# Kernel optimization log

Hardware: AMD Instinct MI355X
Metric: run time of the kernel (lower is better)

## Reference

```python
import jax, jax.numpy as jnp
import numpy as np

N, E, F_IN, H, C = 50000, 800000, 128, 4, 73
HC = H * C  # 292
NEG_SLOPE_ATT = 0.2   # GATv2 attention leaky relu
NEG_SLOPE_ACT = 0.01  # F.leaky_relu default
BN_EPS = 1e-5


def setup_inputs() -> dict:
    key = jax.random.key(0)
    ks = jax.random.split(key, 20)
    rn = lambda k, shp, s=0.05: (jax.random.normal(k, shp, jnp.float32) * s)
    inp = {
        'x': jax.random.normal(ks[0], (N, F_IN), jnp.float32),
        'edge_index': jax.random.randint(ks[1], (2, E), 0, N, jnp.int64),
        # conv1 (in=F_IN)
        'Wl1': rn(ks[2], (HC, F_IN)), 'bl1': rn(ks[3], (HC,)),
        'Wr1': rn(ks[4], (HC, F_IN)), 'br1': rn(ks[5], (HC,)),
        'att1': rn(ks[6], (H, C)), 'b1': rn(ks[7], (HC,)),
        # conv2 (in=HC)
        'Wl2': rn(ks[8], (HC, HC)), 'bl2': rn(ks[9], (HC,)),
        'Wr2': rn(ks[10], (HC, HC)), 'br2': rn(ks[11], (HC,)),
        'att2': rn(ks[12], (H, C)), 'b2': rn(ks[13], (HC,)),
        # shared BatchNorm1d(HC)
        'gamma': jnp.ones((HC,), jnp.float32), 'beta': jnp.zeros((HC,), jnp.float32),
        # classifier Linear(HC, 2)
        'Wc': rn(ks[14], (2, HC)), 'bc': rn(ks[15], (2,)),
    }
    return inp


def _gatv2(x, src, dst, Wl, bl, Wr, br, att, b):
    # lin_l on source, lin_r on target (PyG GATv2Conv, share_weights=False)
    xl = (x @ Wl.T + bl).reshape(-1, H, C)  # [N,H,C]
    xr = (x @ Wr.T + br).reshape(-1, H, C)
    f = xl[src] + xr[dst]                    # [E,H,C] edge-wise gather
    s = jnp.einsum('ehc,hc->eh', jax.nn.leaky_relu(f, NEG_SLOPE_ATT), att)
    # segment softmax over incoming edges of each destination node
    m = jax.ops.segment_max(s, dst, num_segments=N)
    ex = jnp.exp(s - m[dst])
    den = jax.ops.segment_sum(ex, dst, num_segments=N)
    alpha = ex / (den[dst] + 1e-16)          # [E,H]
    out = jax.ops.segment_sum(alpha[:, :, None] * xl[src], dst, num_segments=N)
    return out.reshape(-1, HC) + b           # concat heads + bias


def _bn(x, gamma, beta):
    mu = jnp.mean(x, axis=0)
    var = jnp.mean((x - mu) ** 2, axis=0)
    return (x - mu) * jax.lax.rsqrt(var + BN_EPS) * gamma + beta


def reference(x, edge_index, Wl1, bl1, Wr1, br1, att1, b1,
              Wl2, bl2, Wr2, br2, att2, b2, gamma, beta, Wc, bc):
    src, dst = edge_index[0], edge_index[1]
    h = _gatv2(x, src, dst, Wl1, bl1, Wr1, br1, att1, b1)
    h = jax.nn.leaky_relu(_bn(h, gamma, beta), NEG_SLOPE_ACT)
    h = _gatv2(h, src, dst, Wl2, bl2, Wr2, br2, att2, b2)
    h = jax.nn.leaky_relu(_bn(h, gamma, beta), NEG_SLOPE_ACT)
    return h @ Wc.T + bc
```

## Files before the change

kernel.cpp:

```cpp
#include <hip/hip_runtime.h>

#define HCDIM 292
#define NHEAD 4
#define CDIM 73
#define SLOTS 5
#define NPERM 320
#define BN_EPS 1e-5f
#define LOG2E 1.44269504f

using u16x8 = __attribute__((ext_vector_type(8))) unsigned short;
using f32x4 = __attribute__((ext_vector_type(4))) float;
using u16x4 = __attribute__((ext_vector_type(4))) unsigned short;
using hf2   = __attribute__((ext_vector_type(2))) _Float16;
using v2h   = __attribute__((ext_vector_type(2))) __fp16;
using v8h   = __attribute__((ext_vector_type(8))) __fp16;

__device__ inline v2h pkrtz(float a, float b) {
  return __builtin_amdgcn_cvt_pkrtz(a, b);
}
__device__ inline float fdot2(hf2 a, hf2 b, float c) {
  return __builtin_amdgcn_fdot2(__builtin_bit_cast(v2h, a),
                                __builtin_bit_cast(v2h, b), c, false);
}
__device__ inline ushort f2h(float f) {
  _Float16 h = (_Float16)f;
  return __builtin_bit_cast(ushort, h);
}
__device__ inline float h2f(ushort v) {
  return (float)__builtin_bit_cast(_Float16, v);
}
__device__ inline hf2 habs2(hf2 a) {
  unsigned u = __builtin_bit_cast(unsigned, a) & 0x7fff7fffu;
  return __builtin_bit_cast(hf2, u);
}
__device__ inline float fexp2(float x) {
  float r;
  asm("v_exp_f32 %0, %1" : "=v"(r) : "v"(x));
  return r;
}

#define FMAMIX_LO(ACC, W, U)                                                  \
  asm("v_fma_mix_f32 %0, %1, %2, %0 op_sel_hi:[1,0,0]"                        \
      : "+v"(ACC) : "v"(U), "v"(W))
#define FMAMIX_HI(ACC, W, U)                                                  \
  asm("v_fma_mix_f32 %0, %1, %2, %0 op_sel:[1,0,0] op_sel_hi:[1,0,0]"         \
      : "+v"(ACC) : "v"(U), "v"(W))

__device__ inline float dpp16_allsum(float v) {
  union { float f; int i; } a, b;
  a.f = v;
  b.i = __builtin_amdgcn_update_dpp(0, a.i, 0xB1, 0xf, 0xf, true);
  a.f += b.f;
  b.i = __builtin_amdgcn_update_dpp(0, a.i, 0x4E, 0xf, 0xf, true);
  a.f += b.f;
  b.i = __builtin_amdgcn_update_dpp(0, a.i, 0x124, 0xf, 0xf, true);
  a.f += b.f;
  b.i = __builtin_amdgcn_update_dpp(0, a.i, 0x128, 0xf, 0xf, true);
  a.f += b.f;
  return a.f;
}

__device__ inline int perm2feat(int p, bool& valid) {
  int h, c;
  if (p < 256) {
    h = p >> 6;
    c = ((p & 3) << 4) | ((p >> 2) & 15);
    valid = true;
  } else {
    int q = p - 256;
    h = q >> 4;
    c = 64 + (q & 15);
    valid = (q & 15) < (CDIM - 64);
  }
  return h * CDIM + c;
}

__global__ __launch_bounds__(320) void k_prep(
    const float* __restrict__ Wl1, const float* __restrict__ bl1,
    const float* __restrict__ Wr1, const float* __restrict__ br1,
    const float* __restrict__ Wl2, const float* __restrict__ bl2,
    const float* __restrict__ Wr2, const float* __restrict__ br2,
    ushort* __restrict__ wb1, float* __restrict__ pb1,
    ushort* __restrict__ wb2, float* __restrict__ pb2,
    const float* __restrict__ att1, const float* __restrict__ b1v,
    const float* __restrict__ att2, const float* __restrict__ b2v,
    const float* __restrict__ gamma, const float* __restrict__ beta,
    const float* __restrict__ Wc, float* __restrict__ vecp,
    const int* __restrict__ dst, int* __restrict__ deg, int E) {
  int bx = blockIdx.x, t = threadIdx.x;
  if (bx >= 5 * NPERM) {
    int i = (bx - 5 * NPERM) * 320 + t;
    int i4 = i * 4;
    if (i4 + 3 < E) {
      int4 d = *(const int4*)(dst + i4);
      atomicAdd(&deg[d.x], 1);
      atomicAdd(&deg[d.y], 1);
      atomicAdd(&deg[d.z], 1);
      atomicAdd(&deg[d.w], 1);
    } else {
      for (int k = i4; k < E; ++k) atomicAdd(&deg[dst[k]], 1);
    }
    return;
  }
  int seg = bx / NPERM;
  int p = bx - seg * NPERM;
  bool pv;
  int gn = perm2feat(p, pv);
  if (seg == 4) {
    if (t < 8) {
      const float* src;
      switch (t) {
        case 0: src = att1; break;
        case 1: src = b1v; break;
        case 2: src = att2; break;
        case 3: src = b2v; break;
        case 4: src = gamma; break;
        case 5: src = beta; break;
        case 6: src = Wc; break;
        default: src = Wc + HCDIM; break;
      }
      vecp[t * NPERM + p] = pv ? src[gn] : 0.f;
    }
    return;
  }
  const float* W;
  const float* b;
  ushort* Wp;
  float* pb;
  int Kin, Kpad, kperm;
  if (seg < 2) {
    Kin = 128; Kpad = 128; kperm = 0;
    W = seg ? Wr1 : Wl1; b = seg ? br1 : bl1;
    Wp = wb1 + (size_t)seg * NPERM * 128; pb = pb1 + seg * NPERM;
  } else {
    Kin = HCDIM; Kpad = NPERM; kperm = 1;
    int s2 = seg - 2;
    W = s2 ? Wr2 : Wl2; b = s2 ? br2 : bl2;
    Wp = wb2 + (size_t)s2 * NPERM * NPERM; pb = pb2 + s2 * NPERM;
  }
  if (t < Kpad) {
    int gk = t;
    bool kv = t < Kin;
    if (kperm) { bool v2; gk = perm2feat(t, v2); kv = v2; }
    ushort v = 0;
    if (pv && kv) v = f2h(W[(size_t)gn * Kin + gk]);
    Wp[(size_t)p * Kpad + t] = v;
  }
  if (t == 0) pb[p] = pv ? b[gn] : 0.f;
}

__global__ __launch_bounds__(256) void k_scan_lb(const int* __restrict__ deg,
                                                 unsigned* __restrict__ st,
                                                 int* __restrict__ row_ptr,
                                                 int* __restrict__ cursor,
                                                 int n, int E) {
  __shared__ int s[256];
  __shared__ int sprefix;
  int bid = blockIdx.x, t = threadIdx.x;
  int i = bid * 256 + t;
  int v = (i < n) ? deg[i] : 0;
  s[t] = v;
  __syncthreads();
  for (int off = 1; off < 256; off <<= 1) {
    int tv = (t >= off) ? s[t - off] : 0;
    __syncthreads();
    s[t] += tv;
    __syncthreads();
  }
  if (t == 0) {
    unsigned total = (unsigned)s[255];
    __hip_atomic_store(&st[bid], (1u << 30) | total, __ATOMIC_RELEASE,
                       __HIP_MEMORY_SCOPE_AGENT);
    unsigned run = 0;
    int p = bid - 1;
    while (p >= 0) {
      unsigned x;
      do {
        x = __hip_atomic_load(&st[p], __ATOMIC_ACQUIRE, __HIP_MEMORY_SCOPE_AGENT);
        if (x == 0u) __builtin_amdgcn_s_sleep(1);
      } while (x == 0u);
      run += x & 0x3FFFFFFFu;
      if ((x >> 30) == 2u) break;
      --p;
    }
    __hip_atomic_store(&st[bid], (2u << 30) | (run + total), __ATOMIC_RELEASE,
                       __HIP_MEMORY_SCOPE_AGENT);
    sprefix = (int)run;
  }
  __syncthreads();
  int run = sprefix;
  if (i < n) {
    int rp = run + s[t] - v;
    row_ptr[i] = rp;
    cursor[i] = rp;
  }
  if (i == 0) row_ptr[n] = E;
}

template <int KS, int MODE, int FILL, int ROWS>
__global__ __launch_bounds__(256, 4) void k_gemm_a_lds(
    const void* __restrict__ Av, const ushort* __restrict__ Wb,
    const float* __restrict__ pb, const float* __restrict__ bnsum,
    const float* __restrict__ bnsq, const float* __restrict__ gp,
    const float* __restrict__ btp, float invN, ushort* __restrict__ o0,
    ushort* __restrict__ o1, int M,
    const int* __restrict__ srcs, const int* __restrict__ dsts,
    int* __restrict__ cursor, int* __restrict__ csr_src, int E, int gemmb) {
  if (FILL && (int)blockIdx.x >= gemmb) {
    int i = ((int)blockIdx.x - gemmb) * 256 + (int)threadIdx.x;
    int i4 = i * 4;
    if (i4 + 3 < E) {
      int4 s = *(const int4*)(srcs + i4);
      int4 d = *(const int4*)(dsts + i4);
      csr_src[atomicAdd(&cursor[d.x], 1)] = s.x;
      csr_src[atomicAdd(&cursor[d.y], 1)] = s.y;
      csr_src[atomicAdd(&cursor[d.z], 1)] = s.z;
      csr_src[atomicAdd(&cursor[d.w], 1)] = s.w;
    } else {
      for (int k = i4; k < E; ++k) {
        int pos = atomicAdd(&cursor[dsts[k]], 1);
        csr_src[pos] = srcs[k];
      }
    }
    return;
  }
  constexpr int KSTEPS = KS / 32;
  constexpr int STR = KS + 8;
  constexpr int MI = ROWS / 16;
  __shared__ ushort As[ROWS * STR];
  __shared__ float sScale[MODE ? NPERM : 1];
  __shared__ float sShift[MODE ? NPERM : 1];
  const int tid = threadIdx.x;
  const int rbase = blockIdx.x * ROWS;
  const int wave = tid >> 6, lane = tid & 63;
  const int quad = lane >> 4, lr = lane & 15;
  const int ct = wave;

  if constexpr (MODE == 0) {
    const float* X = (const float*)Av;
    constexpr int NIT = (ROWS * KS / 16) / 256;
#pragma unroll
    for (int k = 0; k < NIT; ++k) {
      int idx = tid + k * 256;
      int row = idx >> 3, sg = idx & 7;
      int gr = rbase + row;
      if (gr >= M) gr = M - 1;
      const float4* p = (const float4*)(X + (size_t)gr * KS + sg * 16);
      float4 f0 = p[0], f1 = p[1], f2 = p[2], f3 = p[3];
      union { v2h h[4]; u16x8 v; } a, b;
      a.h[0] = pkrtz(f0.x, f0.y); a.h[1] = pkrtz(f0.z, f0.w);
      a.h[2] = pkrtz(f1.x, f1.y); a.h[3] = pkrtz(f1.z, f1.w);
      b.h[0] = pkrtz(f2.x, f2.y); b.h[1] = pkrtz(f2.z, f2.w);
      b.h[2] = pkrtz(f3.x, f3.y); b.h[3] = pkrtz(f3.z, f3.w);
      *(u16x8*)(As + row * STR + sg * 16) = a.v;
      *(u16x8*)(As + row * STR + sg * 16 + 8) = b.v;
    }
  } else {
    for (int c = tid; c < NPERM; c += 256) {
      float mu = bnsum[c] * invN;
      float var = bnsq[c] * invN - mu * mu;
      float sc = rsqrtf(var + BN_EPS) * gp[c];
      sScale[c] = sc;
      sShift[c] = btp[c] - mu * sc;
    }
    __syncthreads();
    const ushort* Hn = (const ushort*)Av;
    constexpr int NIT = (ROWS * KS / 8) / 256;
#pragma unroll
    for (int k = 0; k < NIT; ++k) {
      int idx = tid + k * 256;
      int row = idx / (KS / 8), c8 = idx - row * (KS / 8);
      int gr = rbase + row;
      if (gr >= M) gr = M - 1;
      u16x8 v = *(const u16x8*)(Hn + (size_t)gr * KS + c8 * 8);
      int c = c8 * 8;
      float4 s0 = *(const float4*)(sScale + c);
      float4 s1 = *(const float4*)(sScale + c + 4);
      float4 t0 = *(const float4*)(sShift + c);
      float4 t1 = *(const float4*)(sShift + c + 4);
      float f[8];
      f[0] = fmaf(h2f(v[0]), s0.x, t0.x);
      f[1] = fmaf(h2f(v[1]), s0.y, t0.y);
      f[2] = fmaf(h2f(v[2]), s0.z, t0.z);
      f[3] = fmaf(h2f(v[3]), s0.w, t0.w);
      f[4] = fmaf(h2f(v[4]), s1.x, t1.x);
      f[5] = fmaf(h2f(v[5]), s1.y, t1.y);
      f[6] = fmaf(h2f(v[6]), s1.z, t1.z);
      f[7] = fmaf(h2f(v[7]), s1.w, t1.w);
#pragma unroll
      for (int j = 0; j < 8; ++j) f[j] = (f[j] > 0.f) ? f[j] : 0.01f * f[j];
      union { v2h h4[4]; u16x8 o; } u;
#pragma unroll
      for (int j = 0; j < 4; ++j) u.h4[j] = pkrtz(f[2 * j], f[2 * j + 1]);
      *(u16x8*)(As + row * STR + c8 * 8) = u.o;
    }
  }
  __syncthreads();

  const ushort* arow[MI];
#pragma unroll
  for (int i = 0; i < MI; ++i) arow[i] = As + (i * 16 + lr) * STR;

#pragma unroll
  for (int y = 0; y < 2; ++y) {
    const ushort* bcol[5];
#pragma unroll
    for (int i = 0; i < 5; ++i)
      bcol[i] = Wb + (size_t)(y * 320 + ct * 80 + i * 16 + lr) * KS;

    f32x4 acc[MI][5] = {};
    v8h bfb[2][5];
#pragma unroll
    for (int i = 0; i < 5; ++i)
      bfb[0][i] = *(const v8h*)(bcol[i] + quad * 8);
#pragma unroll
    for (int s = 0; s < KSTEPS; ++s) {
      if (s + 1 < KSTEPS) {
#pragma unroll
        for (int i = 0; i < 5; ++i)
          bfb[(s + 1) & 1][i] = *(const v8h*)(bcol[i] + (s + 1) * 32 + quad * 8);
      }
      v8h af[MI];
#pragma unroll
      for (int i = 0; i < MI; ++i)
        af[i] = *(const v8h*)(arow[i] + s * 32 + quad * 8);
#pragma unroll
      for (int ni = 0; ni < 5; ++ni)
#pragma unroll
        for (int mi = 0; mi < MI; ++mi)
          acc[mi][ni] = __builtin_amdgcn_mfma_f32_16x16x32_f16(
              bfb[s & 1][ni], af[mi], acc[mi][ni], 0, 0, 0);
    }

    ushort* out = y ? o1 : o0;
    const int colbase = ct * 80;
    float4 pbv[5];
#pragma unroll
    for (int ni = 0; ni < 5; ++ni)
      pbv[ni] = *(const float4*)(pb + y * 320 + ct * 80 + ni * 16 + quad * 4);
#pragma unroll
    for (int mi = 0; mi < MI; ++mi) {
      int gm = rbase + mi * 16 + lr;
      if (gm >= M) continue;
      ushort* orow = out + (size_t)gm * NPERM + colbase + quad * 4;
#pragma unroll
      for (int ni = 0; ni < 5; ++ni) {
        union { v2h h[2]; u16x4 o; } u;
        u.h[0] = pkrtz(acc[mi][ni][0] + pbv[ni].x, acc[mi][ni][1] + pbv[ni].y);
        u.h[1] = pkrtz(acc[mi][ni][2] + pbv[ni].z, acc[mi][ni][3] + pbv[ni].w);
        *(u16x4*)(orow + ni * 16) = u.o;
      }
    }
  }
}

__global__ __launch_bounds__(128) void k_agg(const ushort* __restrict__ xl,
                                             const ushort* __restrict__ xr,
                                             const int* __restrict__ csr_src,
                                             const int* __restrict__ row_ptr,
                                             const float* __restrict__ attp,
                                             const float* __restrict__ bp,
                                             ushort* __restrict__ out, int n) {
  int wave = threadIdx.x >> 6, lane = threadIdx.x & 63;
  int d = blockIdx.x * 2 + wave;
  if (d >= n) return;
  int start = __builtin_amdgcn_readfirstlane(row_ptr[d]);
  int end = __builtin_amdgcn_readfirstlane(row_ptr[d + 1]);

  float4 bp4 = *(const float4*)(bp + lane * 4);
  float bp5 = bp[256 + lane];

  if (start >= end) {
    union { v2h h[2]; u16x4 o; } u;
    u.h[0] = pkrtz(bp4.x, bp4.y);
    u.h[1] = pkrtz(bp4.z, bp4.w);
    *(u16x4*)(out + (size_t)d * NPERM + lane * 4) = u.o;
    out[(size_t)d * NPERM + 256 + lane] = f2h(bp5);
    return;
  }

  const float C = 0.4f * LOG2E;
  float4 at4 = *(const float4*)(attp + lane * 4);
  hf2 av01{(_Float16)(C * at4.x), (_Float16)(C * at4.y)};
  hf2 av23{(_Float16)(C * at4.z), (_Float16)(C * at4.w)};
  hf2 av5{(_Float16)(C * attp[256 + lane]), (_Float16)0.f};

  hf2 xr01, xr23, xr5;
  {
    uint2 rr = *(const uint2*)(xr + (size_t)d * NPERM + lane * 4);
    xr01 = __builtin_bit_cast(hf2, rr.x);
    xr23 = __builtin_bit_cast(hf2, rr.y);
    xr5 = hf2{__builtin_bit_cast(_Float16, xr[(size_t)d * NPERM + 256 + lane]),
              (_Float16)0.f};
  }
  float Tb = fdot2(xr01, av01, fdot2(xr23, av23, fdot2(xr5, av5, 0.f)));
  Tb = dpp16_allsum(Tb);
  float prv = 1.5f * Tb;
  float acc[SLOTS] = {};
  float den = 0.f;
  int dg = end - start;
  int nfull = dg >> 2;
  int rem = dg & 3;

  uint2 s8[4];
  ushort s1[4];
#pragma unroll
  for (int k = 0; k < 4; ++k) {
    int e = start + k;
    if (e > end - 1) e = end - 1;
    int s = __builtin_amdgcn_readfirstlane(csr_src[e]);
    s8[k] = *(const uint2*)(xl + (size_t)s * NPERM + lane * 4);
    s1[k] = xl[(size_t)s * NPERM + 256 + lane];
  }

  for (int g = 0; g < nfull; ++g) {
    int ebase = start + g * 4 + 4;
    uint2 n8[4];
    ushort n1[4];
#pragma unroll
    for (int k = 0; k < 4; ++k) {
      int e = ebase + k;
      if (e > end - 1) e = end - 1;
      int s = __builtin_amdgcn_readfirstlane(csr_src[e]);
      n8[k] = *(const uint2*)(xl + (size_t)s * NPERM + lane * 4);
      n1[k] = xl[(size_t)s * NPERM + 256 + lane];
    }

    float z[4];
#pragma unroll
    for (int k = 0; k < 4; ++k) {
      hf2 x01 = __builtin_bit_cast(hf2, s8[k].x);
      hf2 x23 = __builtin_bit_cast(hf2, s8[k].y);
      hf2 x5{__builtin_bit_cast(_Float16, s1[k]), (_Float16)0.f};
      float T = fdot2(habs2(x01 + xr01), av01,
                fdot2(habs2(x23 + xr23), av23,
                fdot2(habs2(x5 + xr5), av5, 0.f)));
      float Tl = fdot2(x01, av01, fdot2(x23, av23, fdot2(x5, av5, 0.f)));
      z[k] = fmaf(1.5f, Tl, T);
    }
#pragma unroll
    for (int k = 0; k < 4; ++k) z[k] = dpp16_allsum(z[k]);
    float w[4];
#pragma unroll
    for (int k = 0; k < 4; ++k) {
      w[k] = fexp2(fminf(z[k] + prv, 80.f));
      den += w[k];
    }
#pragma unroll
    for (int k = 0; k < 4; ++k) {
      unsigned ux = s8[k].x, uy = s8[k].y, u5 = (unsigned)s1[k];
      FMAMIX_LO(acc[0], w[k], ux);
      FMAMIX_HI(acc[1], w[k], ux);
      FMAMIX_LO(acc[2], w[k], uy);
      FMAMIX_HI(acc[3], w[k], uy);
      FMAMIX_LO(acc[4], w[k], u5);
    }
#pragma unroll
    for (int k = 0; k < 4; ++k) { s8[k] = n8[k]; s1[k] = n1[k]; }
  }

#pragma unroll
  for (int k = 0; k < 3; ++k) {
    if (k < rem) {
      hf2 x01 = __builtin_bit_cast(hf2, s8[k].x);
      hf2 x23 = __builtin_bit_cast(hf2, s8[k].y);
      hf2 x5{__builtin_bit_cast(_Float16, s1[k]), (_Float16)0.f};
      float T = fdot2(habs2(x01 + xr01), av01,
                fdot2(habs2(x23 + xr23), av23,
                fdot2(habs2(x5 + xr5), av5, 0.f)));
      float Tl = fdot2(x01, av01, fdot2(x23, av23, fdot2(x5, av5, 0.f)));
      float z = fmaf(1.5f, Tl, T);
      z = dpp16_allsum(z);
      float w = fexp2(fminf(z + prv, 80.f));
      den += w;
      unsigned ux = s8[k].x, uy = s8[k].y, u5 = (unsigned)s1[k];
      FMAMIX_LO(acc[0], w, ux);
      FMAMIX_HI(acc[1], w, ux);
      FMAMIX_LO(acc[2], w, uy);
      FMAMIX_HI(acc[3], w, uy);
      FMAMIX_LO(acc[4], w, u5);
    }
  }

  float inv = 1.f / (den + 1e-16f);
  union { v2h h[2]; u16x4 o; } u;
  u.h[0] = pkrtz(fmaf(acc[0], inv, bp4.x), fmaf(acc[1], inv, bp4.y));
  u.h[1] = pkrtz(fmaf(acc[2], inv, bp4.z), fmaf(acc[3], inv, bp4.w));
  *(u16x4*)(out + (size_t)d * NPERM + lane * 4) = u.o;
  out[(size_t)d * NPERM + 256 + lane] = f2h(fmaf(acc[4], inv, bp5));
}

__global__ __launch_bounds__(320) void k_bn_reduce(const ushort* __restrict__ h,
                                                   float* __restrict__ colsum,
                                                   float* __restrict__ colsq,
                                                   int n, int rows_per_block) {
  int c = threadIdx.x;
  int r0 = blockIdx.x * rows_per_block;
  int r1 = min(r0 + rows_per_block, n);
  float s = 0.f, s2 = 0.f;
  for (int r = r0; r < r1; ++r) {
    float v = h2f(h[(size_t)r * NPERM + c]);
    s += v;
    s2 += v * v;
  }
  atomicAdd(&colsum[c], s);
  atomicAdd(&colsq[c], s2);
}

__global__ __launch_bounds__(256) void k_bn_classifier(
    const ushort* __restrict__ h, const float* __restrict__ bnsum,
    const float* __restrict__ bnsq, const float* __restrict__ gp,
    const float* __restrict__ btp, float invN, const float* __restrict__ wc0,
    const float* __restrict__ wc1, const float* __restrict__ bc,
    float* __restrict__ out, int n) {
  int wave = threadIdx.x >> 6, lane = threadIdx.x & 63;
  int r = blockIdx.x * 4 + wave;
  if (r >= n) return;
  float a0 = 0.f, a1 = 0.f;
#pragma unroll
  for (int k = 0; k < SLOTS; ++k) {
    int slot = lane + 64 * k;
    float mu = bnsum[slot] * invN;
    float var = bnsq[slot] * invN - mu * mu;
    float sc = rsqrtf(var + BN_EPS) * gp[slot];
    float sh = btp[slot] - mu * sc;
    float v = fmaf(h2f(h[(size_t)r * NPERM + slot]), sc, sh);
    v = (v > 0.f) ? v : 0.01f * v;
    a0 = fmaf(v, wc0[slot], a0);
    a1 = fmaf(v, wc1[slot], a1);
  }
#pragma unroll
  for (int off = 32; off > 0; off >>= 1) {
    a0 += __shfl_xor(a0, off, 64);
    a1 += __shfl_xor(a1, off, 64);
  }
  if (lane == 0) {
    out[(size_t)2 * r] = a0 + bc[0];
    out[(size_t)2 * r + 1] = a1 + bc[1];
  }
}

extern "C" void kernel_launch(void* const* d_in, const int* in_sizes, int n_in,
                              void* d_out, int out_size, void* d_ws, size_t ws_size,
                              hipStream_t stream) {
  const float* x      = (const float*)d_in[0];
  const int*   eidx   = (const int*)d_in[1];
  const float* Wl1    = (const float*)d_in[2];
  const float* bl1    = (const float*)d_in[3];
  const float* Wr1    = (const float*)d_in[4];
  const float* br1    = (const float*)d_in[5];
  const float* att1   = (const float*)d_in[6];
  const float* b1     = (const float*)d_in[7];
  const float* Wl2    = (const float*)d_in[8];
  const float* bl2    = (const float*)d_in[9];
  const float* Wr2    = (const float*)d_in[10];
  const float* br2    = (const float*)d_in[11];
  const float* att2   = (const float*)d_in[12];
  const float* b2     = (const float*)d_in[13];
  const float* gamma  = (const float*)d_in[14];
  const float* beta   = (const float*)d_in[15];
  const float* Wc     = (const float*)d_in[16];
  const float* bc     = (const float*)d_in[17];
  float* out = (float*)d_out;

  const int FIN = 128;
  const int N = in_sizes[0] / FIN;
  const int E = in_sizes[1] / 2;

  const int* src = eidx;
  const int* dst = eidx + E;

  ushort* h      = (ushort*)d_ws;
  ushort* xl     = h + (size_t)N * NPERM;
  ushort* xr     = xl + (size_t)N * NPERM;
  ushort* wb1    = xr + (size_t)N * NPERM;
  ushort* wb2    = wb1 + (size_t)2 * NPERM * 128;
  float* pb1     = (float*)(wb2 + (size_t)2 * NPERM * NPERM);
  float* pb2     = pb1 + 2 * NPERM;
  float* vecp    = pb2 + 2 * NPERM;
  int* row_ptr   = (int*)(vecp + 8 * NPERM);
  int* cursor    = row_ptr + N + 1;
  int* csr_src   = cursor + N;
  int* deg       = csr_src + E;
  unsigned* scanst = (unsigned*)(deg + N);
  int* tickets   = (int*)(scanst + 256);
  float* colsum1 = (float*)(tickets + 4);
  float* colsq1  = colsum1 + NPERM;
  float* colsum2 = colsq1 + NPERM;
  float* colsq2  = colsum2 + NPERM;
  const size_t zero_bytes = (size_t)(N + 256 + 4 + 4 * NPERM) * 4;

  const int G = (N + 255) / 256;
  const int AGGB = (N + 3) / 4;
  const int AGG2 = (N + 1) / 2;
  const int GEMMB = (N + 31) / 32;
  const int FB = (E + 1023) / 1024;
  const int HISTB = (E + 1279) / 1280;

  const float* att1p = vecp;
  const float* b1p   = vecp + NPERM;
  const float* att2p = vecp + 2 * NPERM;
  const float* b2p   = vecp + 3 * NPERM;
  const float* gp    = vecp + 4 * NPERM;
  const float* btp   = vecp + 5 * NPERM;
  const float* wc0   = vecp + 6 * NPERM;
  const float* wc1   = vecp + 7 * NPERM;

  const int BNB = 1024;
  const int RPB = (N + BNB - 1) / BNB;
  const float invN = 1.f / (float)N;

  hipMemsetAsync(deg, 0, zero_bytes, stream);
  k_prep<<<5 * NPERM + HISTB, 320, 0, stream>>>(
      Wl1, bl1, Wr1, br1, Wl2, bl2, Wr2, br2, wb1, pb1, wb2, pb2,
      att1, b1, att2, b2, gamma, beta, Wc, vecp, dst, deg, E);
  k_scan_lb<<<G, 256, 0, stream>>>(deg, scanst, row_ptr, cursor, N, E);
  k_gemm_a_lds<128, 0, 1, 32><<<GEMMB + FB, 256, 0, stream>>>(
      (const void*)x, wb1, pb1, nullptr, nullptr, nullptr, nullptr, 0.f,
      xl, xr, N, src, dst, cursor, csr_src, E, GEMMB);
  k_agg<<<AGG2, 128, 0, stream>>>(xl, xr, csr_src, row_ptr, att1p, b1p, h, N);
  k_bn_reduce<<<BNB, NPERM, 0, stream>>>(h, colsum1, colsq1, N, RPB);
  k_gemm_a_lds<NPERM, 1, 0, 32><<<GEMMB, 256, 0, stream>>>(
      (const void*)h, wb2, pb2, colsum1, colsq1, gp, btp, invN,
      xl, xr, N, nullptr, nullptr, nullptr, nullptr, 0, GEMMB);
  k_agg<<<AGG2, 128, 0, stream>>>(xl, xr, csr_src, row_ptr, att2p, b2p, h, N);
  k_bn_reduce<<<BNB, NPERM, 0, stream>>>(h, colsum2, colsq2, N, RPB);
  k_bn_classifier<<<AGGB, 256, 0, stream>>>(h, colsum2, colsq2, gp, btp, invN,
                                            wc0, wc1, bc, out, N);
}
```

Baseline: 611.2 us.

## Parallelize scan lookback across a wavefront and enlarge GEMM row tiles

The decoupled-lookback scan now has a whole wavefront inspect 64 predecessor blocks at once, using a ballot and a shuffle reduction, instead of one thread walking back serially. The GEMM kernels move from 32 to 64 rows per block, with the occupancy hint lowered to 3 and a scheduling barrier placed after the A-fragment loads. Larger tiles reuse each B fragment over more rows and halve the block count, at the cost of more registers per thread and fewer resident waves.

```diff
diff --git a/kernel.cpp b/kernel.cpp
--- a/kernel.cpp
+++ b/kernel.cpp
@@ -167,25 +167,48 @@
     s[t] += tv;
     __syncthreads();
   }
-  if (t == 0) {
-    unsigned total = (unsigned)s[255];
+  unsigned total = (unsigned)s[255];
+  if (t == 0)
     __hip_atomic_store(&st[bid], (1u << 30) | total, __ATOMIC_RELEASE,
                        __HIP_MEMORY_SCOPE_AGENT);
+  if (t < 64) {
     unsigned run = 0;
-    int p = bid - 1;
-    while (p >= 0) {
-      unsigned x;
-      do {
-        x = __hip_atomic_load(&st[p], __ATOMIC_ACQUIRE, __HIP_MEMORY_SCOPE_AGENT);
-        if (x == 0u) __builtin_amdgcn_s_sleep(1);
-      } while (x == 0u);
-      run += x & 0x3FFFFFFFu;
-      if ((x >> 30) == 2u) break;
-      --p;
-    }
-    __hip_atomic_store(&st[bid], (2u << 30) | (run + total), __ATOMIC_RELEASE,
-                       __HIP_MEMORY_SCOPE_AGENT);
-    sprefix = (int)run;
+    int base = bid - 1;
+    bool done = (bid == 0);
+    while (!done) {
+      int p = base - t;
+      unsigned myv = 0;
+      int stat = 2;
+      if (p >= 0) {
+        unsigned x;
+        do {
+          x = __hip_atomic_load(&st[p], __ATOMIC_ACQUIRE,
+                                __HIP_MEMORY_SCOPE_AGENT);
+          if (x == 0u) __builtin_amdgcn_s_sleep(1);
+        } while (x == 0u);
+        myv = x & 0x3FFFFFFFu;
+        stat = (int)(x >> 30);
+      }
+      unsigned long long m = __ballot(stat == 2);
+      unsigned contrib;
+      if (m) {
+        int fi = __ffsll((long long)m) - 1;
+        contrib = (t <= fi) ? myv : 0u;
+        done = true;
+      } else {
+        contrib = myv;
+        base -= 64;
+      }
+#pragma unroll
+      for (int off = 32; off > 0; off >>= 1)
+        contrib += (unsigned)__shfl_xor((int)contrib, off, 64);
+      run += contrib;
+    }
+    if (t == 0) {
+      __hip_atomic_store(&st[bid], (2u << 30) | (run + total), __ATOMIC_RELEASE,
+                         __HIP_MEMORY_SCOPE_AGENT);
+      sprefix = (int)run;
+    }
   }
   __syncthreads();
   int run = sprefix;
@@ -198,7 +221,7 @@
 }
 
 template <int KS, int MODE, int FILL, int ROWS>
-__global__ __launch_bounds__(256, 4) void k_gemm_a_lds(
+__global__ __launch_bounds__(256, 3) void k_gemm_a_lds(
     const void* __restrict__ Av, const ushort* __restrict__ Wb,
     const float* __restrict__ pb, const float* __restrict__ bnsum,
     const float* __restrict__ bnsq, const float* __restrict__ gp,
@@ -324,6 +347,7 @@
 #pragma unroll
       for (int i = 0; i < MI; ++i)
         af[i] = *(const v8h*)(arow[i] + s * 32 + quad * 8);
+      __builtin_amdgcn_sched_barrier(0x7);
 #pragma unroll
       for (int ni = 0; ni < 5; ++ni)
 #pragma unroll
@@ -593,7 +617,7 @@
   const int G = (N + 255) / 256;
   const int AGGB = (N + 3) / 4;
   const int AGG2 = (N + 1) / 2;
-  const int GEMMB = (N + 31) / 32;
+  const int GEMMB = (N + 63) / 64;
   const int FB = (E + 1023) / 1024;
   const int HISTB = (E + 1279) / 1280;
 
@@ -615,12 +639,12 @@
       Wl1, bl1, Wr1, br1, Wl2, bl2, Wr2, br2, wb1, pb1, wb2, pb2,
       att1, b1, att2, b2, gamma, beta, Wc, vecp, dst, deg, E);
   k_scan_lb<<<G, 256, 0, stream>>>(deg, scanst, row_ptr, cursor, N, E);
-  k_gemm_a_lds<128, 0, 1, 32><<<GEMMB + FB, 256, 0, stream>>>(
+  k_gemm_a_lds<128, 0, 1, 64><<<GEMMB + FB, 256, 0, stream>>>(
       (const void*)x, wb1, pb1, nullptr, nullptr, nullptr, nullptr, 0.f,
       xl, xr, N, src, dst, cursor, csr_src, E, GEMMB);
   k_agg<<<AGG2, 128, 0, stream>>>(xl, xr, csr_src, row_ptr, att1p, b1p, h, N);
   k_bn_reduce<<<BNB, NPERM, 0, stream>>>(h, colsum1, colsq1, N, RPB);
-  k_gemm_a_lds<NPERM, 1, 0, 32><<<GEMMB, 256, 0, stream>>>(
+  k_gemm_a_lds<NPERM, 1, 0, 64><<<GEMMB, 256, 0, stream>>>(
       (const void*)h, wb2, pb2, colsum1, colsq1, gp, btp, invN,
       xl, xr, N, nullptr, nullptr, nullptr, nullptr, 0, GEMMB);
   k_agg<<<AGG2, 128, 0, stream>>>(xl, xr, csr_src, row_ptr, att2p, b2p, h, N);
```

After: 542.0 us, median of 2. 1.13x faster.
